# Optimization experiments

Measured on AMD Instinct MI355X. Metric: run time of the kernel, lower is better.

The kernel has to match this reference:

```python
import jax, jax.numpy as jnp
import numpy as np

L, D, H, HID, V, MAXLEN = 4, 768, 12, 3072, 32000, 1024
HD = D // H

def _pe_table(max_len, d_model):
    pos = np.arange(max_len)[:, None].astype(np.float64)
    i = np.arange(d_model)[None, :]
    ang = pos / np.power(10000.0, 2 * (i // 2) / d_model)
    ang[:, 0::2] = np.sin(ang[:, 0::2])
    ang[:, 1::2] = np.cos(ang[:, 1::2])
    return jnp.asarray(ang, dtype=jnp.float32)

def _layernorm(x, g, b, eps=1e-5):
    mu = jnp.mean(x, axis=-1, keepdims=True)
    var = jnp.mean(jnp.square(x - mu), axis=-1, keepdims=True)
    return (x - mu) * jax.lax.rsqrt(var + eps) * g + b

def setup_inputs() -> dict:
    key = jax.random.key(0)
    ks = jax.random.split(key, 16)
    s = 0.02
    inp = {
        'tokens': jax.random.randint(ks[0], (4, 1024), 0, V),
        'emb': jax.random.normal(ks[1], (V, D), jnp.float32) * s,
        'pe': _pe_table(MAXLEN, D),
        'ln1_g': jnp.ones((L, D), jnp.float32), 'ln1_b': jnp.zeros((L, D), jnp.float32),
        'wq': jax.random.normal(ks[2], (L, D, D), jnp.float32) * s, 'bq': jnp.zeros((L, D), jnp.float32),
        'wk': jax.random.normal(ks[3], (L, D, D), jnp.float32) * s, 'bk': jnp.zeros((L, D), jnp.float32),
        'wv': jax.random.normal(ks[4], (L, D, D), jnp.float32) * s, 'bv': jnp.zeros((L, D), jnp.float32),
        'wo': jax.random.normal(ks[5], (L, D, D), jnp.float32) * s, 'bo': jnp.zeros((L, D), jnp.float32),
        'ln2_g': jnp.ones((L, D), jnp.float32), 'ln2_b': jnp.zeros((L, D), jnp.float32),
        'w1': jax.random.normal(ks[6], (L, D, HID), jnp.float32) * s, 'b1': jnp.zeros((L, HID), jnp.float32),
        'w2': jax.random.normal(ks[7], (L, HID, D), jnp.float32) * s, 'b2': jnp.zeros((L, D), jnp.float32),
        'lnf_g': jnp.ones((D,), jnp.float32), 'lnf_b': jnp.zeros((D,), jnp.float32),
        'w_out': jax.random.normal(ks[8], (D, V), jnp.float32) * s,
    }
    return inp

def reference(tokens, emb, pe, ln1_g, ln1_b, wq, bq, wk, bk, wv, bv, wo, bo, ln2_g, ln2_b, w1, b1, w2, b2, lnf_g, lnf_b, w_out):
    B, S = tokens.shape
    x = emb[tokens] + pe[:S]  # [B,S,D]
    causal = jnp.tril(jnp.ones((S, S), bool))  # True = keep
    scale = 1.0 / jnp.sqrt(jnp.float32(D))  # NOTE: module scales by sqrt(d_model), not sqrt(head_dim)
    for l in range(L):
        h = _layernorm(x, ln1_g[l], ln1_b[l])
        def heads(w, b):
            return (h @ w + b).reshape(B, S, H, HD).transpose(0, 2, 1, 3)  # [B,H,S,HD]
        q, k, v = heads(wq[l], bq[l]), heads(wk[l], bk[l]), heads(wv[l], bv[l])
        scores = jnp.einsum('bhqd,bhkd->bhqk', q, k) * scale
        scores = jnp.where(causal, scores, -jnp.inf)
        probs = jax.nn.softmax(scores, axis=-1)
        attn = jnp.einsum('bhqk,bhkd->bhqd', probs, v)
        attn = attn.transpose(0, 2, 1, 3).reshape(B, S, D)
        x = x + attn @ wo[l] + bo[l]
        h2 = _layernorm(x, ln2_g[l], ln2_b[l])
        x = x + jax.nn.relu(h2 @ w1[l] + b1[l]) @ w2[l] + b2[l]
    hs = _layernorm(x, lnf_g, lnf_b)
    return hs @ w_out  # [B,S,V]
```

## Files before the change

kernel.cpp:

```cpp
#include <hip/hip_runtime.h>


typedef __bf16 bf16_t;
typedef bf16_t bf16x8 __attribute__((ext_vector_type(8)));
typedef float f32x4 __attribute__((ext_vector_type(4)));

#define GLD16(G, L) __builtin_amdgcn_global_load_lds(                          \
    (const __attribute__((address_space(1))) unsigned int*)(const void*)(G),   \
    (__attribute__((address_space(3))) unsigned int*)(void*)(L), 16, 0, 0)

__device__ __forceinline__ f32x4 mfma16(bf16x8 a, bf16x8 b, f32x4 c) {
  return __builtin_amdgcn_mfma_f32_16x16x32_bf16(a, b, c, 0, 0, 0);
}

__device__ __forceinline__ void barrier_raw() {
  asm volatile("s_barrier" ::: "memory");
}

#define RED16_MAX(x) { x = fmaxf(x, __shfl_xor(x, 1)); x = fmaxf(x, __shfl_xor(x, 2)); \
                       x = fmaxf(x, __shfl_xor(x, 4)); x = fmaxf(x, __shfl_xor(x, 8)); }
#define RED16_SUM(x) { x += __shfl_xor(x, 1); x += __shfl_xor(x, 2); \
                       x += __shfl_xor(x, 4); x += __shfl_xor(x, 8); }

__device__ __forceinline__ int SW64(int row, int col) {
  return row * 64 + (col ^ ((row & 7) << 3));
}

__global__ __launch_bounds__(256)
void tconv_k(const float* __restrict__ in, bf16_t* __restrict__ out, int K, int N,
             size_t in_ls, size_t out_ls) {
  __shared__ float tile[32][33];
  in  += (size_t)blockIdx.z * in_ls;
  out += (size_t)blockIdx.z * out_ls;
  const int n0 = blockIdx.x * 32, k0 = blockIdx.y * 32;
  const int tx = threadIdx.x & 31, ty = threadIdx.x >> 5;
#pragma unroll
  for (int j = 0; j < 4; ++j)
    tile[ty + j * 8][tx] = in[(size_t)(k0 + ty + j * 8) * N + n0 + tx];
  __syncthreads();
#pragma unroll
  for (int j = 0; j < 4; ++j)
    out[(size_t)(n0 + ty + j * 8) * K + k0 + tx] = (bf16_t)tile[tx][ty + j * 8];
}

__global__ void qkvbias_k(const float* __restrict__ bq, const float* __restrict__ bk,
                          const float* __restrict__ bv, float* __restrict__ out) {
  const int l = blockIdx.x;
  for (int j = threadIdx.x; j < 2304; j += 256) {
    float v = (j < 768) ? bq[l * 768 + j]
            : (j < 1536) ? bk[l * 768 + j - 768]
                         : bv[l * 768 + j - 1536];
    out[l * 2304 + j] = v;
  }
}

__global__ __launch_bounds__(256)
void embed_k(const int* __restrict__ tok, const float* __restrict__ emb,
             const float* __restrict__ pe, float* __restrict__ xf) {
  const int row = blockIdx.x, tid = threadIdx.x;
  const int s = row & 1023;
  const int t = tok[row];
  float* o = xf + (size_t)row * 768;
  const float* e = emb + (size_t)t * 768;
  const float* p = pe + (size_t)s * 768;
  o[tid]       = e[tid]       + p[tid];
  o[tid + 256] = e[tid + 256] + p[tid + 256];
  o[tid + 512] = e[tid + 512] + p[tid + 512];
}

__global__ __launch_bounds__(256)
void ln_k(const float* __restrict__ x, const float* __restrict__ g,
          const float* __restrict__ bb, bf16_t* __restrict__ out) {
  const int row = blockIdx.x, tid = threadIdx.x;
  const int wave = tid >> 6, lane = tid & 63;
  const float* xr = x + (size_t)row * 768;
  float v0 = xr[tid], v1 = xr[tid + 256], v2 = xr[tid + 512];
  float s = v0 + v1 + v2;
  __shared__ float red[4];
#pragma unroll
  for (int off = 32; off; off >>= 1) s += __shfl_xor(s, off);
  if (lane == 0) red[wave] = s;
  __syncthreads();
  const float mu = (red[0] + red[1] + red[2] + red[3]) * (1.0f / 768.0f);
  const float d0 = v0 - mu, d1 = v1 - mu, d2 = v2 - mu;
  float s2 = d0 * d0 + d1 * d1 + d2 * d2;
#pragma unroll
  for (int off = 32; off; off >>= 1) s2 += __shfl_xor(s2, off);
  __syncthreads();
  if (lane == 0) red[wave] = s2;
  __syncthreads();
  const float rstd = rsqrtf((red[0] + red[1] + red[2] + red[3]) * (1.0f / 768.0f) + 1e-5f);
  bf16_t* orow = out + (size_t)row * 768;
  orow[tid]       = (bf16_t)(d0 * rstd * g[tid]       + bb[tid]);
  orow[tid + 256] = (bf16_t)(d1 * rstd * g[tid + 256] + bb[tid + 256]);
  orow[tid + 512] = (bf16_t)(d2 * rstd * g[tid + 512] + bb[tid + 512]);
}

template <bool BIAS, bool RELU, bool OUTF32, bool NT>
__global__ __launch_bounds__(512, 2)
void gemm8p(const bf16_t* __restrict__ A, const bf16_t* __restrict__ BT,
            const float* __restrict__ bias,
            float* __restrict__ outF, bf16_t* __restrict__ outB,
            int M, int N, int K) {
  extern __shared__ char smem[];
  const int NT_TILES = K >> 6;
  const int tilesM = M >> 8;
  const int cpx = gridDim.x >> 3;
  const int blk = ((int)blockIdx.x & 7) * cpx + ((int)blockIdx.x >> 3);
  const int tm = blk % tilesM, tn = blk / tilesM;
  const int tid = threadIdx.x;
  const int lane = tid & 63, wave = tid >> 6;
  const int wr = wave >> 2, wc = wave & 3;
  const int lrow = lane & 15, koct = lane >> 4;

  const size_t rowK = (size_t)K * 2;
  const int srow = tid >> 3;
  const int cswz = ((tid & 7) ^ (srow & 7)) << 4;
  const char* gA = (const char*)(A + (size_t)tm * 256 * K) + (size_t)srow * rowK + cswz;
  const char* gB = (const char*)(BT + (size_t)tn * 256 * K) + (size_t)srow * rowK + cswz;

  const int swz = (lrow & 7) << 4;
  const int aB0 = (wr * 128 + lrow) * 128 + ((koct * 16) ^ swz);
  const int bB0 = 32768 + (wc * 64 + lrow) * 128 + ((koct * 16) ^ swz);

  auto stageA = [&](int t) {
    char* d = smem + ((t & 1) << 16);
    const size_t kb = (size_t)t * 128;
    GLD16(gA + kb,              d + tid * 16);
    GLD16(gA + 64 * rowK + kb,  d + 8192 + tid * 16);
    GLD16(gA + 128 * rowK + kb, d + 16384 + tid * 16);
    GLD16(gA + 192 * rowK + kb, d + 24576 + tid * 16);
  };
  auto stageB = [&](int t) {
    char* d = smem + ((t & 1) << 16) + 32768;
    const size_t kb = (size_t)t * 128;
    GLD16(gB + kb,              d + tid * 16);
    GLD16(gB + 64 * rowK + kb,  d + 8192 + tid * 16);
    GLD16(gB + 128 * rowK + kb, d + 16384 + tid * 16);
    GLD16(gB + 192 * rowK + kb, d + 24576 + tid * 16);
  };

  stageA(0); stageB(0);
  stageA(1); stageB(1);

  f32x4 acc[8][4] = {};

  for (int t = 0; t < NT_TILES; ++t) {
    const char* rb = smem + ((t & 1) << 16);
    const bool pf = (t + 2) < NT_TILES;
    if (t == NT_TILES - 1) asm volatile("s_waitcnt vmcnt(0)" ::: "memory");
    else                   asm volatile("s_waitcnt vmcnt(8)" ::: "memory");
    barrier_raw();

    bf16x8 a0[4][2], a1[4][2], b[4][2];
#pragma unroll
    for (int mi = 0; mi < 4; ++mi) {
      const int o = aB0 + mi * 2048;
      a0[mi][0] = *(const bf16x8*)(rb + o);
      a0[mi][1] = *(const bf16x8*)(rb + (o ^ 64));
    }
#pragma unroll
    for (int ni = 0; ni < 2; ++ni) {
      const int o = bB0 + ni * 2048;
      b[ni][0] = *(const bf16x8*)(rb + o);
      b[ni][1] = *(const bf16x8*)(rb + (o ^ 64));
    }
    barrier_raw();
    __builtin_amdgcn_s_setprio(1);
#pragma unroll
    for (int mi = 0; mi < 4; ++mi)
#pragma unroll
      for (int ni = 0; ni < 2; ++ni) {
        acc[mi][ni] = mfma16(a0[mi][0], b[ni][0], acc[mi][ni]);
        acc[mi][ni] = mfma16(a0[mi][1], b[ni][1], acc[mi][ni]);
      }
    __builtin_amdgcn_s_setprio(0);
    barrier_raw();

#pragma unroll
    for (int ni = 2; ni < 4; ++ni) {
      const int o = bB0 + ni * 2048;
      b[ni][0] = *(const bf16x8*)(rb + o);
      b[ni][1] = *(const bf16x8*)(rb + (o ^ 64));
    }
    __builtin_amdgcn_s_setprio(1);
#pragma unroll
    for (int mi = 0; mi < 4; ++mi)
#pragma unroll
      for (int ni = 2; ni < 4; ++ni) {
        acc[mi][ni] = mfma16(a0[mi][0], b[ni][0], acc[mi][ni]);
        acc[mi][ni] = mfma16(a0[mi][1], b[ni][1], acc[mi][ni]);
      }
    __builtin_amdgcn_s_setprio(0);
    asm volatile("s_waitcnt lgkmcnt(0)" ::: "memory");
    barrier_raw();

    if (pf) stageB(t + 2);
#pragma unroll
    for (int mi = 0; mi < 4; ++mi) {
      const int o = aB0 + (mi + 4) * 2048;
      a1[mi][0] = *(const bf16x8*)(rb + o);
      a1[mi][1] = *(const bf16x8*)(rb + (o ^ 64));
    }
    __builtin_amdgcn_s_setprio(1);
#pragma unroll
    for (int mi = 0; mi < 4; ++mi)
#pragma unroll
      for (int ni = 0; ni < 2; ++ni) {
        acc[mi + 4][ni] = mfma16(a1[mi][0], b[ni][0], acc[mi + 4][ni]);
        acc[mi + 4][ni] = mfma16(a1[mi][1], b[ni][1], acc[mi + 4][ni]);
      }
    __builtin_amdgcn_s_setprio(0);
    asm volatile("s_waitcnt lgkmcnt(0)" ::: "memory");
    barrier_raw();

    if (pf) stageA(t + 2);
    __builtin_amdgcn_s_setprio(1);
#pragma unroll
    for (int mi = 0; mi < 4; ++mi)
#pragma unroll
      for (int ni = 2; ni < 4; ++ni) {
        acc[mi + 4][ni] = mfma16(a1[mi][0], b[ni][0], acc[mi + 4][ni]);
        acc[mi + 4][ni] = mfma16(a1[mi][1], b[ni][1], acc[mi + 4][ni]);
      }
    __builtin_amdgcn_s_setprio(0);
  }

  const int row0 = tm * 256 + wr * 128, col0 = tn * 256 + wc * 64;
#pragma unroll
  for (int ni = 0; ni < 4; ++ni) {
    const int col = col0 + ni * 16 + lrow;
    const float bv = BIAS ? bias[col] : 0.0f;
#pragma unroll
    for (int mi = 0; mi < 8; ++mi) {
#pragma unroll
      for (int r = 0; r < 4; ++r) {
        const int row = row0 + mi * 16 + koct * 4 + r;
        float v = acc[mi][ni][r] + bv;
        if (RELU) v = fmaxf(v, 0.0f);
        const size_t idx = (size_t)row * N + col;
        if (OUTF32) {
          if (NT) __builtin_nontemporal_store(v, &outF[idx]);
          else    outF[idx] = v;
        } else {
          outB[idx] = (bf16_t)v;
        }
      }
    }
  }
}

template <bool BIAS, bool RELU, bool RESID, bool OUTF32>
__global__ __launch_bounds__(256, 2)
void gemmS(const bf16_t* __restrict__ A, const bf16_t* __restrict__ BT,
           const float* __restrict__ bias, const float* __restrict__ resid,
           float* __restrict__ outF, bf16_t* __restrict__ outB,
           int M, int N, int K) {
  extern __shared__ char smem[];
  const int NT = K >> 6;
  const int tiles_n = N >> 7;
  const int tm = blockIdx.x / tiles_n, tn = blockIdx.x % tiles_n;
  const int tid = threadIdx.x;
  const int wave = tid >> 6, lane = tid & 63;
  const int wr = wave >> 1, wc = wave & 1;
  const int lrow = lane & 15, koct = lane >> 4;

  const char* gA[2];
  const char* gB[4];
  {
    const char* Ab = (const char*)(A + (size_t)tm * 64 * K);
    const char* Bb = (const char*)(BT + (size_t)tn * 128 * K);
#pragma unroll
    for (int i = 0; i < 2; ++i) {
      const int off = i * 4096 + tid * 16;
      const int row = off >> 7;
      const int src = off ^ ((row & 7) << 4);
      gA[i] = Ab + (size_t)row * (2 * K) + (src & 127);
    }
#pragma unroll
    for (int i = 0; i < 4; ++i) {
      const int off = i * 4096 + tid * 16;
      const int row = off >> 7;
      const int src = off ^ ((row & 7) << 4);
      gB[i] = Bb + (size_t)row * (2 * K) + (src & 127);
    }
  }

  int aoff[2][2], boff[2][4];
#pragma unroll
  for (int kk = 0; kk < 2; ++kk) {
#pragma unroll
    for (int mi = 0; mi < 2; ++mi) {
      const int row = wr * 32 + mi * 16 + lrow;
      aoff[kk][mi] = (row * 128 + kk * 64 + koct * 16) ^ ((lrow & 7) << 4);
    }
#pragma unroll
    for (int ni = 0; ni < 4; ++ni) {
      const int row = wc * 64 + ni * 16 + lrow;
      boff[kk][ni] = 8192 + ((row * 128 + kk * 64 + koct * 16) ^ ((lrow & 7) << 4));
    }
  }

#pragma unroll
  for (int t = 0; t < 2; ++t) {
    char* sb = smem + t * 24576;
    const size_t kb = (size_t)t * 128;
    GLD16(gA[0] + kb, sb + tid * 16);
    GLD16(gA[1] + kb, sb + 4096 + tid * 16);
    GLD16(gB[0] + kb, sb + 8192 + tid * 16);
    GLD16(gB[1] + kb, sb + 12288 + tid * 16);
    GLD16(gB[2] + kb, sb + 16384 + tid * 16);
    GLD16(gB[3] + kb, sb + 20480 + tid * 16);
  }

  f32x4 acc[2][4] = {};

  for (int t = 0; t < NT; ++t) {
    char* sb = smem + (t % 3) * 24576;
    char* sb2 = smem + ((t + 2) % 3) * 24576;
    const bool pf = (t + 2) < NT;
    const size_t kb2 = (size_t)(t + 2) * 128;

    if (t == NT - 1) asm volatile("s_waitcnt vmcnt(0)" ::: "memory");
    else             asm volatile("s_waitcnt vmcnt(6)" ::: "memory");
    barrier_raw();

#pragma unroll
    for (int kk = 0; kk < 2; ++kk) {
      bf16x8 af[2], bfr[4];
#pragma unroll
      for (int mi = 0; mi < 2; ++mi)
        af[mi] = *(const bf16x8*)(sb + aoff[kk][mi]);
#pragma unroll
      for (int ni = 0; ni < 4; ++ni)
        bfr[ni] = *(const bf16x8*)(sb + boff[kk][ni]);
      if (pf) {
        if (kk == 0) {
          GLD16(gA[0] + kb2, sb2 + tid * 16);
          GLD16(gA[1] + kb2, sb2 + 4096 + tid * 16);
          GLD16(gB[0] + kb2, sb2 + 8192 + tid * 16);
        } else {
          GLD16(gB[1] + kb2, sb2 + 12288 + tid * 16);
          GLD16(gB[2] + kb2, sb2 + 16384 + tid * 16);
          GLD16(gB[3] + kb2, sb2 + 20480 + tid * 16);
        }
      }
      barrier_raw();
      __builtin_amdgcn_s_setprio(1);
#pragma unroll
      for (int mi = 0; mi < 2; ++mi)
#pragma unroll
        for (int ni = 0; ni < 4; ++ni)
          acc[mi][ni] = mfma16(af[mi], bfr[ni], acc[mi][ni]);
      __builtin_amdgcn_s_setprio(0);
    }
  }

  const int row0 = tm * 64 + wr * 32, col0 = tn * 128 + wc * 64;
#pragma unroll
  for (int ni = 0; ni < 4; ++ni) {
    const int col = col0 + ni * 16 + lrow;
    const float bv = BIAS ? bias[col] : 0.0f;
#pragma unroll
    for (int mi = 0; mi < 2; ++mi) {
#pragma unroll
      for (int r = 0; r < 4; ++r) {
        const int row = row0 + mi * 16 + koct * 4 + r;
        float v = acc[mi][ni][r] + bv;
        if (RELU) v = fmaxf(v, 0.0f);
        const size_t idx = (size_t)row * N + col;
        if (RESID) v += resid[idx];
        if (OUTF32) outF[idx] = v;
        else        outB[idx] = (bf16_t)v;
      }
    }
  }
}

__global__ __launch_bounds__(256)
void attn_k(const bf16_t* __restrict__ qkv, bf16_t* __restrict__ ab) {
  __shared__ __align__(16) bf16_t Qs[64 * 64];
  __shared__ __align__(16) bf16_t Ks[64 * 64];
  __shared__ __align__(16) bf16_t Vt[64 * 64];
  __shared__ __align__(16) bf16_t Ps[4][16 * 64];
  const int qt = blockIdx.x, h = blockIdx.y, b = blockIdx.z;
  const int tid = threadIdx.x;
  const int wave = tid >> 6, lane = tid & 63;
  const int lrow = lane & 15, koct = lane >> 4;
  const float scale = 0.03608439182435161f;

  const size_t RS = 2304;
  const bf16_t* qbase = qkv + h * 64;
  const bf16_t* kbase = qkv + 768 + h * 64;
  const bf16_t* vbase = qkv + 1536 + h * 64;

  const int sr = tid >> 3;
  const int sc = (((tid & 7) ^ (sr & 7)) << 3);

  {
#pragma unroll
    for (int i = 0; i < 2; ++i)
      GLD16(qbase + (size_t)(b * 1024 + qt * 64 + i * 32 + sr) * RS + sc,
            Qs + i * 2048 + tid * 8);
  }
  __syncthreads();
  bf16x8 qf[2];
  qf[0] = *(const bf16x8*)&Qs[SW64(wave * 16 + lrow, koct * 8)];
  qf[1] = *(const bf16x8*)&Qs[SW64(wave * 16 + lrow, 32 + koct * 8)];

  float m_r[4], l_r[4];
  f32x4 o[4] = {};
#pragma unroll
  for (int r = 0; r < 4; ++r) { m_r[r] = -1e30f; l_r[r] = 0.0f; }

  for (int kt = 0; kt <= qt; ++kt) {
    __syncthreads();
    {
#pragma unroll
      for (int i = 0; i < 2; ++i)
        GLD16(kbase + (size_t)(b * 1024 + kt * 64 + i * 32 + sr) * RS + sc,
              Ks + i * 2048 + tid * 8);
    }
    {
      const int kvr = lane;
      const int d0 = wave * 16;
      const bf16_t* vr = vbase + (size_t)(b * 1024 + kt * 64 + kvr) * RS + d0;
      bf16x8 v0 = *(const bf16x8*)vr;
      bf16x8 v1 = *(const bf16x8*)(vr + 8);
#pragma unroll
      for (int j = 0; j < 8; ++j) {
        Vt[(d0 + j) * 64 + (kvr ^ (j << 3))]     = v0[j];
        Vt[(d0 + 8 + j) * 64 + (kvr ^ (j << 3))] = v1[j];
      }
    }
    __syncthreads();

    f32x4 s[4] = {};
#pragma unroll
    for (int ni = 0; ni < 4; ++ni) {
      bf16x8 kf0 = *(const bf16x8*)&Ks[SW64(ni * 16 + lrow, koct * 8)];
      bf16x8 kf1 = *(const bf16x8*)&Ks[SW64(ni * 16 + lrow, 32 + koct * 8)];
      s[ni] = mfma16(qf[0], kf0, s[ni]);
      s[ni] = mfma16(qf[1], kf1, s[ni]);
    }

    const int qrow = qt * 64 + wave * 16 + koct * 4;
    float rm[4];
#pragma unroll
    for (int r = 0; r < 4; ++r) rm[r] = -1e30f;
#pragma unroll
    for (int ni = 0; ni < 4; ++ni) {
      const int kcol = kt * 64 + ni * 16 + lrow;
#pragma unroll
      for (int r = 0; r < 4; ++r) {
        float v = s[ni][r] * scale;
        if (kcol > qrow + r) v = -1e30f;
        s[ni][r] = v;
        rm[r] = fmaxf(rm[r], v);
      }
    }
#pragma unroll
    for (int r = 0; r < 4; ++r) RED16_MAX(rm[r]);
    float corr[4], ps[4];
#pragma unroll
    for (int r = 0; r < 4; ++r) {
      const float mn = fmaxf(m_r[r], rm[r]);
      corr[r] = __expf(m_r[r] - mn);
      m_r[r] = mn;
      ps[r] = 0.0f;
    }
#pragma unroll
    for (int ni = 0; ni < 4; ++ni)
#pragma unroll
      for (int r = 0; r < 4; ++r) {
        const float p = __expf(s[ni][r] - m_r[r]);
        s[ni][r] = p;
        ps[r] += p;
      }
#pragma unroll
    for (int r = 0; r < 4; ++r) RED16_SUM(ps[r]);
#pragma unroll
    for (int r = 0; r < 4; ++r) l_r[r] = l_r[r] * corr[r] + ps[r];
#pragma unroll
    for (int ni = 0; ni < 4; ++ni)
#pragma unroll
      for (int r = 0; r < 4; ++r) o[ni][r] *= corr[r];

#pragma unroll
    for (int ni = 0; ni < 4; ++ni)
#pragma unroll
      for (int r = 0; r < 4; ++r) {
        const int prow = koct * 4 + r;
        Ps[wave][prow * 64 + ((ni * 16 + lrow) ^ ((prow & 7) << 3))] =
            (bf16_t)s[ni][r];
      }
    __syncthreads();

    bf16x8 pa0 = *(const bf16x8*)&Ps[wave][SW64(lrow, koct * 8)];
    bf16x8 pa1 = *(const bf16x8*)&Ps[wave][SW64(lrow, 32 + koct * 8)];
#pragma unroll
    for (int ni = 0; ni < 4; ++ni) {
      bf16x8 vf0 = *(const bf16x8*)&Vt[SW64(ni * 16 + lrow, koct * 8)];
      bf16x8 vf1 = *(const bf16x8*)&Vt[SW64(ni * 16 + lrow, 32 + koct * 8)];
      o[ni] = mfma16(pa0, vf0, o[ni]);
      o[ni] = mfma16(pa1, vf1, o[ni]);
    }
  }

#pragma unroll
  for (int r = 0; r < 4; ++r) {
    const float inv = 1.0f / l_r[r];
    const int row = qt * 64 + wave * 16 + koct * 4 + r;
#pragma unroll
    for (int ni = 0; ni < 4; ++ni)
      ab[(size_t)(b * 1024 + row) * 768 + h * 64 + ni * 16 + lrow] =
          (bf16_t)(o[ni][r] * inv);
  }
}

extern "C" void kernel_launch(void* const* d_in, const int* in_sizes, int n_in,
                              void* d_out, int out_size, void* d_ws, size_t ws_size,
                              hipStream_t stream) {
  (void)in_sizes; (void)n_in; (void)out_size; (void)ws_size;
  const int*   tok   = (const int*)d_in[0];
  const float* emb   = (const float*)d_in[1];
  const float* pe    = (const float*)d_in[2];
  const float* ln1_g = (const float*)d_in[3];
  const float* ln1_b = (const float*)d_in[4];
  const float* wq    = (const float*)d_in[5];
  const float* bq    = (const float*)d_in[6];
  const float* wk    = (const float*)d_in[7];
  const float* bk    = (const float*)d_in[8];
  const float* wv    = (const float*)d_in[9];
  const float* bv    = (const float*)d_in[10];
  const float* wo    = (const float*)d_in[11];
  const float* bo    = (const float*)d_in[12];
  const float* ln2_g = (const float*)d_in[13];
  const float* ln2_b = (const float*)d_in[14];
  const float* w1    = (const float*)d_in[15];
  const float* b1    = (const float*)d_in[16];
  const float* w2    = (const float*)d_in[17];
  const float* b2    = (const float*)d_in[18];
  const float* lnf_g = (const float*)d_in[19];
  const float* lnf_b = (const float*)d_in[20];
  const float* w_out = (const float*)d_in[21];
  float* out = (float*)d_out;

  char* ws = (char*)d_ws;
  size_t off = 0;
  auto alloc = [&](size_t bytes) -> void* {
    void* p = ws + off;
    off += (bytes + 255) & ~(size_t)255;
    return p;
  };
  float*  xf      = (float*)alloc(4096ull * 768 * 4);
  bf16_t* hb      = (bf16_t*)alloc(4096ull * 768 * 2);
  bf16_t* qkvb    = (bf16_t*)alloc(4096ull * 2304 * 2);
  bf16_t* ab      = (bf16_t*)alloc(4096ull * 768 * 2);
  bf16_t* fb      = (bf16_t*)alloc(4096ull * 3072 * 2);
  float*  qkvbias = (float*)alloc(4ull * 2304 * 4);
  bf16_t* wqkvT   = (bf16_t*)alloc(4ull * 2304 * 768 * 2);
  bf16_t* woT     = (bf16_t*)alloc(4ull * 768 * 768 * 2);
  bf16_t* w1T     = (bf16_t*)alloc(4ull * 3072 * 768 * 2);
  bf16_t* w2T     = (bf16_t*)alloc(4ull * 768 * 3072 * 2);
  bf16_t* woutT   = (bf16_t*)alloc(32000ull * 768 * 2);

  tconv_k<<<dim3(24, 24, 4), 256, 0, stream>>>(wq, wqkvT, 768, 768,
      768ull * 768, 2304ull * 768);
  tconv_k<<<dim3(24, 24, 4), 256, 0, stream>>>(wk, wqkvT + 768ull * 768, 768, 768,
      768ull * 768, 2304ull * 768);
  tconv_k<<<dim3(24, 24, 4), 256, 0, stream>>>(wv, wqkvT + 2ull * 768 * 768, 768, 768,
      768ull * 768, 2304ull * 768);
  tconv_k<<<dim3(24, 24, 4), 256, 0, stream>>>(wo, woT, 768, 768,
      768ull * 768, 768ull * 768);
  tconv_k<<<dim3(96, 24, 4), 256, 0, stream>>>(w1, w1T, 768, 3072,
      768ull * 3072, 3072ull * 768);
  tconv_k<<<dim3(24, 96, 4), 256, 0, stream>>>(w2, w2T, 3072, 768,
      3072ull * 768, 768ull * 3072);
  tconv_k<<<dim3(1000, 24, 1), 256, 0, stream>>>(w_out, woutT, 768, 32000, 0, 0);
  qkvbias_k<<<4, 256, 0, stream>>>(bq, bk, bv, qkvbias);

  embed_k<<<4096, 256, 0, stream>>>(tok, emb, pe, xf);

  const size_t SMEM8P = 131072;
  const size_t SMEMS  = 3 * 24576;
  for (int l = 0; l < 4; ++l) {
    ln_k<<<4096, 256, 0, stream>>>(xf, ln1_g + l * 768, ln1_b + l * 768, hb);
    gemm8p<true, false, false, false><<<16 * 9, 512, SMEM8P, stream>>>(
        hb, wqkvT + (size_t)l * 2304 * 768, qkvbias + l * 2304,
        nullptr, qkvb, 4096, 2304, 768);
    attn_k<<<dim3(16, 12, 4), 256, 0, stream>>>(qkvb, ab);
    gemmS<true, false, true, true><<<64 * 6, 256, SMEMS, stream>>>(
        ab, woT + (size_t)l * 768 * 768, bo + l * 768,
        xf, xf, nullptr, 4096, 768, 768);
    ln_k<<<4096, 256, 0, stream>>>(xf, ln2_g + l * 768, ln2_b + l * 768, hb);
    gemm8p<true, true, false, false><<<16 * 12, 512, SMEM8P, stream>>>(
        hb, w1T + (size_t)l * 3072 * 768, b1 + l * 3072,
        nullptr, fb, 4096, 3072, 768);
    gemmS<true, false, true, true><<<64 * 6, 256, SMEMS, stream>>>(
        fb, w2T + (size_t)l * 768 * 3072, b2 + l * 768,
        xf, xf, nullptr, 4096, 768, 3072);
  }
  ln_k<<<4096, 256, 0, stream>>>(xf, lnf_g, lnf_b, hb);
  gemm8p<false, false, true, true><<<16 * 125, 512, SMEM8P, stream>>>(
      hb, woutT, nullptr, out, nullptr, 4096, 32000, 768);
}
```

Before: 1.060 ms.

## Stage GEMM epilogue through LDS for vectorized stores and supergroup tile order

The gemm8p epilogue now writes accumulators into a per-wave LDS scratch area and then reads them back as contiguous rows. This lets it issue 16-byte global stores (f32x4 or bf16x8) instead of scattered scalar stores, which targets write efficiency, most of all for the large fp32 logits output. A new SUPER template parameter groups output tiles into bands of 5 N-tiles for the vocab projection, to improve L2 reuse of weight tiles. The extra LDS round trip and barrier add latency to the epilogue.

```diff
diff --git a/kernel.cpp b/kernel.cpp
--- a/kernel.cpp
+++ b/kernel.cpp
@@ -96,7 +96,7 @@
   orow[tid + 512] = (bf16_t)(d2 * rstd * g[tid + 512] + bb[tid + 512]);
 }
 
-template <bool BIAS, bool RELU, bool OUTF32, bool NT>
+template <bool BIAS, bool RELU, bool OUTF32, bool NT, int SUPER>
 __global__ __launch_bounds__(512, 2)
 void gemm8p(const bf16_t* __restrict__ A, const bf16_t* __restrict__ BT,
             const float* __restrict__ bias,
@@ -107,7 +107,16 @@
   const int tilesM = M >> 8;
   const int cpx = gridDim.x >> 3;
   const int blk = ((int)blockIdx.x & 7) * cpx + ((int)blockIdx.x >> 3);
-  const int tm = blk % tilesM, tn = blk / tilesM;
+  int tm, tn;
+  if (SUPER > 0) {
+    const int grp = SUPER * tilesM;
+    const int g = blk / grp, r = blk % grp;
+    tm = r / SUPER;
+    tn = g * SUPER + r % SUPER;
+  } else {
+    tm = blk % tilesM;
+    tn = blk / tilesM;
+  }
   const int tid = threadIdx.x;
   const int lane = tid & 63, wave = tid >> 6;
   const int wr = wave >> 2, wc = wave & 3;
@@ -226,25 +235,61 @@
     __builtin_amdgcn_s_setprio(0);
   }
 
+  barrier_raw();
   const int row0 = tm * 256 + wr * 128, col0 = tn * 256 + wc * 64;
-#pragma unroll
-  for (int ni = 0; ni < 4; ++ni) {
-    const int col = col0 + ni * 16 + lrow;
-    const float bv = BIAS ? bias[col] : 0.0f;
-#pragma unroll
-    for (int mi = 0; mi < 8; ++mi) {
-#pragma unroll
-      for (int r = 0; r < 4; ++r) {
-        const int row = row0 + mi * 16 + koct * 4 + r;
-        float v = acc[mi][ni][r] + bv;
-        if (RELU) v = fmaxf(v, 0.0f);
-        const size_t idx = (size_t)row * N + col;
-        if (OUTF32) {
-          if (NT) __builtin_nontemporal_store(v, &outF[idx]);
-          else    outF[idx] = v;
-        } else {
-          outB[idx] = (bf16_t)v;
-        }
+  float bv[4];
+#pragma unroll
+  for (int ni = 0; ni < 4; ++ni)
+    bv[ni] = BIAS ? bias[col0 + ni * 16 + lrow] : 0.0f;
+
+  if (OUTF32) {
+    float* lf = (float*)smem + wave * (32 * 68);
+#pragma unroll
+    for (int ph = 0; ph < 4; ++ph) {
+#pragma unroll
+      for (int mm = 0; mm < 2; ++mm) {
+        const int mi = ph * 2 + mm;
+#pragma unroll
+        for (int ni = 0; ni < 4; ++ni)
+#pragma unroll
+          for (int r = 0; r < 4; ++r) {
+            float v = acc[mi][ni][r] + bv[ni];
+            if (RELU) v = fmaxf(v, 0.0f);
+            lf[(mm * 16 + koct * 4 + r) * 68 + ni * 16 + lrow] = v;
+          }
+      }
+#pragma unroll
+      for (int j = 0; j < 8; ++j) {
+        const int lr = j * 4 + koct;
+        const int lc = lrow * 4;
+        f32x4 v4 = *(const f32x4*)&lf[lr * 68 + lc];
+        f32x4* dst = (f32x4*)&outF[(size_t)(row0 + ph * 32 + lr) * N + col0 + lc];
+        if (NT) __builtin_nontemporal_store(v4, dst);
+        else    *dst = v4;
+      }
+    }
+  } else {
+    bf16_t* lb = (bf16_t*)smem + wave * (32 * 72);
+#pragma unroll
+    for (int ph = 0; ph < 4; ++ph) {
+#pragma unroll
+      for (int mm = 0; mm < 2; ++mm) {
+        const int mi = ph * 2 + mm;
+#pragma unroll
+        for (int ni = 0; ni < 4; ++ni)
+#pragma unroll
+          for (int r = 0; r < 4; ++r) {
+            float v = acc[mi][ni][r] + bv[ni];
+            if (RELU) v = fmaxf(v, 0.0f);
+            lb[(mm * 16 + koct * 4 + r) * 72 + ni * 16 + lrow] = (bf16_t)v;
+          }
+      }
+#pragma unroll
+      for (int j = 0; j < 4; ++j) {
+        const int lr = j * 8 + (lane >> 3);
+        const int lc = (lane & 7) * 8;
+        bf16x8 v8 = *(const bf16x8*)&lb[lr * 72 + lc];
+        *(bf16x8*)&outB[(size_t)(row0 + ph * 32 + lr) * N + col0 + lc] = v8;
       }
     }
   }
@@ -586,7 +631,7 @@
   const size_t SMEMS  = 3 * 24576;
   for (int l = 0; l < 4; ++l) {
     ln_k<<<4096, 256, 0, stream>>>(xf, ln1_g + l * 768, ln1_b + l * 768, hb);
-    gemm8p<true, false, false, false><<<16 * 9, 512, SMEM8P, stream>>>(
+    gemm8p<true, false, false, false, 0><<<16 * 9, 512, SMEM8P, stream>>>(
         hb, wqkvT + (size_t)l * 2304 * 768, qkvbias + l * 2304,
         nullptr, qkvb, 4096, 2304, 768);
     attn_k<<<dim3(16, 12, 4), 256, 0, stream>>>(qkvb, ab);
@@ -594,7 +639,7 @@
         ab, woT + (size_t)l * 768 * 768, bo + l * 768,
         xf, xf, nullptr, 4096, 768, 768);
     ln_k<<<4096, 256, 0, stream>>>(xf, ln2_g + l * 768, ln2_b + l * 768, hb);
-    gemm8p<true, true, false, false><<<16 * 12, 512, SMEM8P, stream>>>(
+    gemm8p<true, true, false, false, 0><<<16 * 12, 512, SMEM8P, stream>>>(
         hb, w1T + (size_t)l * 3072 * 768, b1 + l * 3072,
         nullptr, fb, 4096, 3072, 768);
     gemmS<true, false, true, true><<<64 * 6, 256, SMEMS, stream>>>(
@@ -602,6 +647,6 @@
         xf, xf, nullptr, 4096, 768, 3072);
   }
   ln_k<<<4096, 256, 0, stream>>>(xf, lnf_g, lnf_b, hb);
-  gemm8p<false, false, true, true><<<16 * 125, 512, SMEM8P, stream>>>(
+  gemm8p<false, false, true, true, 5><<<16 * 125, 512, SMEM8P, stream>>>(
       hb, woutT, nullptr, out, nullptr, 4096, 32000, 768);
 }
```

New measurement: 984.5 us, median of 2. -7.1%, faster.
